# Kernel optimization log

Hardware: AMD Instinct MI355X
Metric: run time of the kernel (lower is better)

Reference implementation:

```python
import jax, jax.numpy as jnp
import numpy as np

KEY_CHANNELS = 256


def conv1x1_relu(x, w, b):
    # x: [B, Cin, H, W], w: [Cout, Cin], b: [Cout] -> [B, Cout, H, W]
    y = jnp.einsum('oc,bchw->bohw', w, x) + b[None, :, None, None]
    return jax.nn.relu(y)


def setup_inputs() -> dict:
    key = jax.random.key(0)
    ks = jax.random.split(key, 16)
    B, C, H, W = 8, 512, 128, 128
    Kc, Kp = KEY_CHANNELS, 150
    sc = lambda cin: 1.0 / np.sqrt(cin)
    return {
        'x': jax.random.normal(ks[0], (B, C, H, W), jnp.float32),
        'proxy': jax.random.normal(ks[1], (B, C, Kp, 1), jnp.float32),
        'w_fp1': jax.random.normal(ks[2], (Kc, C), jnp.float32) * sc(C),
        'b_fp1': jax.random.normal(ks[3], (Kc,), jnp.float32) * 0.1,
        'w_fp2': jax.random.normal(ks[4], (Kc, Kc), jnp.float32) * sc(Kc),
        'b_fp2': jax.random.normal(ks[5], (Kc,), jnp.float32) * 0.1,
        'w_fo1': jax.random.normal(ks[6], (Kc, C), jnp.float32) * sc(C),
        'b_fo1': jax.random.normal(ks[7], (Kc,), jnp.float32) * 0.1,
        'w_fo2': jax.random.normal(ks[8], (Kc, Kc), jnp.float32) * sc(Kc),
        'b_fo2': jax.random.normal(ks[9], (Kc,), jnp.float32) * 0.1,
        'w_fd': jax.random.normal(ks[10], (Kc, C), jnp.float32) * sc(C),
        'b_fd': jax.random.normal(ks[11], (Kc,), jnp.float32) * 0.1,
        'w_fu': jax.random.normal(ks[12], (C, Kc), jnp.float32) * sc(Kc),
        'b_fu': jax.random.normal(ks[13], (C,), jnp.float32) * 0.1,
    }


def reference(x, proxy, w_fp1, b_fp1, w_fp2, b_fp2, w_fo1, b_fo1,
              w_fo2, b_fo2, w_fd, b_fd, w_fu, b_fu):
    B, C, H, W = x.shape
    Kc = w_fp1.shape[0]
    # f_pixel: two 1x1 conv(+folded BN)+ReLU blocks -> query [B, HW, Kc]
    q = conv1x1_relu(conv1x1_relu(x, w_fp1, b_fp1), w_fp2, b_fp2)
    query = q.reshape(B, Kc, H * W).transpose(0, 2, 1)
    # f_object -> key [B, Kc, Kp]
    k = conv1x1_relu(conv1x1_relu(proxy, w_fo1, b_fo1), w_fo2, b_fo2)
    key = k.reshape(B, Kc, -1)
    # f_down -> value [B, Kp, Kc]
    v = conv1x1_relu(proxy, w_fd, b_fd)
    value = v.reshape(B, Kc, -1).transpose(0, 2, 1)
    # cross-attention: softmax(Q K^T / sqrt(Kc)) V
    sim = jnp.einsum('bnc,bck->bnk', query, key) * (Kc ** -0.5)
    sim = jax.nn.softmax(sim, axis=-1)
    context = jnp.einsum('bnk,bkc->bnc', sim, value)  # [B, HW, Kc]
    context = context.transpose(0, 2, 1).reshape(B, Kc, H, W)
    # f_up: 1x1 conv(+folded BN)+ReLU back to in_channels
    return conv1x1_relu(context, w_fu, b_fu)
```

## Files before the change

### kernel.cpp

```cpp
#include <hip/hip_runtime.h>
#include <hip/hip_bf16.h>


typedef __bf16 bf16x8 __attribute__((ext_vector_type(8)));
typedef float f32x4 __attribute__((ext_vector_type(4)));

#define AS1 __attribute__((address_space(1)))
#define AS3 __attribute__((address_space(3)))
#define MFMA_16x16x32(a, b, c) __builtin_amdgcn_mfma_f32_16x16x32_bf16((a), (b), (c), 0, 0, 0)

__device__ __forceinline__ unsigned short f2bf(float f) {
  union { float f; unsigned u; } x; x.f = f;
  unsigned r = (x.u + 0x7FFFu + ((x.u >> 16) & 1u)) >> 16;
  return (unsigned short)r;
}

__global__ __launch_bounds__(256) void cast_weights(
    const float* __restrict__ w1, const float* __restrict__ w2,
    const float* __restrict__ wu, unsigned short* __restrict__ W1b,
    unsigned short* __restrict__ W2b, unsigned short* __restrict__ Wub) {
  int i = blockIdx.x * 256 + threadIdx.x;
  if (i < 131072) W1b[i] = f2bf(w1[i]);
  else if (i < 196608) W2b[i - 131072] = f2bf(w2[i - 131072]);
  else if (i < 327680) Wub[i - 196608] = f2bf(wu[i - 196608]);
}

__global__ __launch_bounds__(256) void kv_kernel(
    const float* __restrict__ proxy,
    const float* __restrict__ w_fo1, const float* __restrict__ b_fo1,
    const float* __restrict__ w_fo2, const float* __restrict__ b_fo2,
    const float* __restrict__ w_fd, const float* __restrict__ b_fd,
    unsigned short* __restrict__ keyT, unsigned short* __restrict__ Vv) {
  __shared__ float cols[512][8];
  __shared__ float k1s[256][8];
  const int b = blockIdx.y;
  const int p0 = blockIdx.x * 8;
  const int t = threadIdx.x;
#pragma unroll
  for (int i = 0; i < 8; i++) {
    int idx = t + i * 256;
    int c = idx >> 2, q = idx & 3;
    int p = p0 + q * 2;
    float2 v = make_float2(0.f, 0.f);
    if (p < 150) v = *(const float2*)(proxy + ((size_t)b * 512 + c) * 150 + p);
    cols[c][q * 2 + 0] = v.x;
    cols[c][q * 2 + 1] = v.y;
  }
  __syncthreads();
  float accV[8], accK[8];
  {
    float bv = b_fd[t], bk = b_fo1[t];
#pragma unroll
    for (int px = 0; px < 8; px++) { accV[px] = bv; accK[px] = bk; }
  }
#define KV_FMA(j, wv_, wk_)                                      \
  { float4 ca = *(const float4*)&cols[c + j][0];                 \
    float4 cb = *(const float4*)&cols[c + j][4];                 \
    accV[0] += wv_ * ca.x; accV[1] += wv_ * ca.y;                \
    accV[2] += wv_ * ca.z; accV[3] += wv_ * ca.w;                \
    accV[4] += wv_ * cb.x; accV[5] += wv_ * cb.y;                \
    accV[6] += wv_ * cb.z; accV[7] += wv_ * cb.w;                \
    accK[0] += wk_ * ca.x; accK[1] += wk_ * ca.y;                \
    accK[2] += wk_ * ca.z; accK[3] += wk_ * ca.w;                \
    accK[4] += wk_ * cb.x; accK[5] += wk_ * cb.y;                \
    accK[6] += wk_ * cb.z; accK[7] += wk_ * cb.w; }
  for (int c = 0; c < 512; c += 4) {
    float4 wv4 = *(const float4*)(w_fd + (size_t)t * 512 + c);
    float4 wk4 = *(const float4*)(w_fo1 + (size_t)t * 512 + c);
    KV_FMA(0, wv4.x, wk4.x)
    KV_FMA(1, wv4.y, wk4.y)
    KV_FMA(2, wv4.z, wk4.z)
    KV_FMA(3, wv4.w, wk4.w)
  }
#pragma unroll
  for (int px = 0; px < 8; px++) {
    Vv[((size_t)b * 256 + t) * 160 + p0 + px] = f2bf(fmaxf(accV[px], 0.f));
    k1s[t][px] = fmaxf(accK[px], 0.f);
  }
  __syncthreads();
  float accY[8];
  {
    float by = b_fo2[t];
#pragma unroll
    for (int px = 0; px < 8; px++) accY[px] = by;
  }
#define KV_FMA2(j, wy_)                                          \
  { float4 ca = *(const float4*)&k1s[c + j][0];                  \
    float4 cb = *(const float4*)&k1s[c + j][4];                  \
    accY[0] += wy_ * ca.x; accY[1] += wy_ * ca.y;                \
    accY[2] += wy_ * ca.z; accY[3] += wy_ * ca.w;                \
    accY[4] += wy_ * cb.x; accY[5] += wy_ * cb.y;                \
    accY[6] += wy_ * cb.z; accY[7] += wy_ * cb.w; }
  for (int c = 0; c < 256; c += 4) {
    float4 wy4 = *(const float4*)(w_fo2 + (size_t)t * 256 + c);
    KV_FMA2(0, wy4.x)
    KV_FMA2(1, wy4.y)
    KV_FMA2(2, wy4.z)
    KV_FMA2(3, wy4.w)
  }
#pragma unroll
  for (int px = 0; px < 8; px++)
    keyT[((size_t)b * 160 + p0 + px) * 256 + t] = f2bf(fmaxf(accY[px], 0.f));
}

__global__ __launch_bounds__(256, 3) void gemm1_fused(
    const float* __restrict__ X, const unsigned short* __restrict__ Bt,
    const float* __restrict__ bias, unsigned short* __restrict__ Cq) {
  const int HW = 16384, K = 512, N = 256;
  __shared__ float Af[64 * 128];
  __shared__ unsigned short Bs[128 * 64];
  const int r = blockIdx.x;
  const int b = blockIdx.y;
  const int my = ((r >> 4) << 3) | (r & 7);
  const int nx = (r >> 3) & 1;
  const int m0 = my * 128, n0 = nx * 128;
  const int tid = threadIdx.x;
  const int w = tid >> 6, l = tid & 63;
  const int lr = l & 15, lg = l >> 4;
  const int wm = (w >> 1) * 64, wn = (w & 1) * 64;
  const float* Xb = X + (size_t)b * K * HW;
  const unsigned short* Btb = Bt + (size_t)n0 * K;
  const f32x4 zero = {0.f, 0.f, 0.f, 0.f};
  f32x4 acc[4][4];
#pragma unroll
  for (int m = 0; m < 4; m++)
#pragma unroll
    for (int n = 0; n < 4; n++) acc[m][n] = zero;

  const int arow = l >> 5, acol = l & 31;
  const int bsub = l >> 3, bcol = (l & 7) * 8;
  for (int kt = 0; kt < K; kt += 64) {
    __syncthreads();
#pragma unroll
    for (int i = 0; i < 8; i++) {
      const int rk = w * 16 + i * 2 + arow;
      const int s = (rk >> 3) & 7;
      __builtin_amdgcn_global_load_lds(
          (AS1 void*)(Xb + (size_t)(kt + rk) * HW + m0 + ((acol ^ s) << 2)),
          (AS3 void*)(Af + (w * 16 + i * 2) * 128), 16, 0, 0);
    }
#pragma unroll
    for (int i = 0; i < 4; i++) {
      __builtin_amdgcn_global_load_lds(
          (AS1 void*)(Btb + (size_t)(w * 32 + i * 8 + bsub) * K + kt + bcol),
          (AS3 void*)(Bs + (w * 32 + i * 8) * 64), 16, 0, 0);
    }
    __syncthreads();
#pragma unroll
    for (int ks = 0; ks < 2; ks++) {
      bf16x8 aF[4], bF[4];
      const int s = ks * 4 + lg;
#pragma unroll
      for (int m = 0; m < 4; m++) {
        const int p = wm + m * 16 + lr;
        const int cb = ((((p >> 2) ^ s) << 2) | (p & 3));
        bf16x8 a;
#pragma unroll
        for (int j = 0; j < 8; j++)
          a[j] = (__bf16)Af[(ks * 32 + lg * 8 + j) * 128 + cb];
        aF[m] = a;
      }
#pragma unroll
      for (int n = 0; n < 4; n++)
        bF[n] = *(const bf16x8*)(Bs + (wn + n * 16 + lr) * 64 + ks * 32 + lg * 8);
#pragma unroll
      for (int m = 0; m < 4; m++)
#pragma unroll
        for (int n = 0; n < 4; n++) acc[m][n] = MFMA_16x16x32(aF[m], bF[n], acc[m][n]);
    }
  }
  unsigned short* Cb = Cq + (size_t)b * HW * N;
#pragma unroll
  for (int m = 0; m < 4; m++) {
#pragma unroll
    for (int n = 0; n < 4; n++) {
      const int col = n0 + wn + n * 16 + lr;
      const float bc = bias[col];
#pragma unroll
      for (int r2 = 0; r2 < 4; r2++) {
        const int row = m0 + wm + m * 16 + lg * 4 + r2;
        Cb[(size_t)row * N + col] = f2bf(fmaxf(acc[m][n][r2] + bc, 0.f));
      }
    }
  }
}

template <int BIAS_ROW, int OUTF32, int COLOC>
__global__ __launch_bounds__(256, 4) void gemm_bt_relu(
    const unsigned short* __restrict__ A, const unsigned short* __restrict__ Bt,
    const float* __restrict__ bias, void* __restrict__ Cout,
    int M, int N, int K, long long sA, long long sB, long long sC) {
  __shared__ unsigned short As[128 * 64];
  __shared__ unsigned short Bs[128 * 64];
  int m0, n0, b;
  if (COLOC == 1) {
    const int g = blockIdx.x, x = g & 7, j = g >> 3;
    const int og = ((j >> 1) << 3) | x;
    n0 = (j & 1) * 128; m0 = (og & 127) * 128; b = og >> 7;
  } else if (COLOC == 2) {
    const int g = blockIdx.x, x = g & 7, j = g >> 3;
    const int og = ((j >> 2) << 3) | x;
    m0 = (j & 3) * 128; n0 = (og & 127) * 128; b = og >> 7;
  } else {
    b = blockIdx.z; m0 = blockIdx.x * 128; n0 = blockIdx.y * 128;
  }
  const int tid = threadIdx.x;
  const int w = tid >> 6, l = tid & 63;
  const int lr = l & 15, lg = l >> 4;
  const int wm = (w >> 1) * 64, wn = (w & 1) * 64;
  const unsigned short* Ab = A + (size_t)b * sA + (size_t)m0 * K;
  const unsigned short* Btb = Bt + (size_t)b * sB + (size_t)n0 * K;
  const f32x4 zero = {0.f, 0.f, 0.f, 0.f};
  f32x4 acc[4][4];
#pragma unroll
  for (int m = 0; m < 4; m++)
#pragma unroll
    for (int n = 0; n < 4; n++) acc[m][n] = zero;

  const int srow = w * 32 + (l >> 3);
  const int scol = (l & 7) * 8;
  for (int kt = 0; kt < K; kt += 64) {
    __syncthreads();
#pragma unroll
    for (int i = 0; i < 4; i++) {
      __builtin_amdgcn_global_load_lds(
          (AS1 void*)(Ab + (size_t)(srow + i * 8) * K + kt + scol),
          (AS3 void*)(As + (w * 32 + i * 8) * 64), 16, 0, 0);
      __builtin_amdgcn_global_load_lds(
          (AS1 void*)(Btb + (size_t)(srow + i * 8) * K + kt + scol),
          (AS3 void*)(Bs + (w * 32 + i * 8) * 64), 16, 0, 0);
    }
    __syncthreads();
#pragma unroll
    for (int ks = 0; ks < 2; ks++) {
      bf16x8 aF[4], bF[4];
#pragma unroll
      for (int m = 0; m < 4; m++)
        aF[m] = *(const bf16x8*)(As + (wm + m * 16 + lr) * 64 + ks * 32 + lg * 8);
#pragma unroll
      for (int n = 0; n < 4; n++)
        bF[n] = *(const bf16x8*)(Bs + (wn + n * 16 + lr) * 64 + ks * 32 + lg * 8);
#pragma unroll
      for (int m = 0; m < 4; m++)
#pragma unroll
        for (int n = 0; n < 4; n++) acc[m][n] = MFMA_16x16x32(aF[m], bF[n], acc[m][n]);
    }
  }
#pragma unroll
  for (int m = 0; m < 4; m++) {
#pragma unroll
    for (int n = 0; n < 4; n++) {
      const int col = n0 + wn + n * 16 + lr;
      const float bc = BIAS_ROW ? 0.f : bias[col];
#pragma unroll
      for (int r = 0; r < 4; r++) {
        const int row = m0 + wm + m * 16 + lg * 4 + r;
        float v = acc[m][n][r] + (BIAS_ROW ? bias[row] : bc);
        v = fmaxf(v, 0.f);
        if (OUTF32)
          ((float*)Cout)[(size_t)b * sC + (size_t)row * N + col] = v;
        else
          ((unsigned short*)Cout)[(size_t)b * sC + (size_t)row * N + col] = f2bf(v);
      }
    }
  }
}

__global__ __launch_bounds__(256, 4) void attn_kernel(
    const unsigned short* __restrict__ Q, const unsigned short* __restrict__ Kt,
    const unsigned short* __restrict__ Vv, unsigned short* __restrict__ ctxT) {
  const int HW = 16384;
  __shared__ unsigned short Pls[128 * 160];
  const int b = blockIdx.y;
  const int pix0 = blockIdx.x * 128;
  const int tid = threadIdx.x;
  const int w = tid >> 6, l = tid & 63;
  const int lr = l & 15, lg = l >> 4;
  const unsigned short* Qb = Q + ((size_t)b * HW + pix0 + w * 32) * 256;
  const unsigned short* Kb = Kt + (size_t)b * 160 * 256;
  const unsigned short* Vb = Vv + (size_t)b * 256 * 160;
  const f32x4 zero = {0.f, 0.f, 0.f, 0.f};

  f32x4 acc[2][10];
#pragma unroll
  for (int m = 0; m < 2; m++)
#pragma unroll
    for (int n = 0; n < 10; n++) acc[m][n] = zero;
#pragma unroll 2
  for (int ks = 0; ks < 8; ks++) {
    bf16x8 aF[2];
#pragma unroll
    for (int m = 0; m < 2; m++)
      aF[m] = *(const bf16x8*)(Qb + (size_t)(m * 16 + lr) * 256 + ks * 32 + lg * 8);
#pragma unroll
    for (int n = 0; n < 10; n++) {
      bf16x8 bF = *(const bf16x8*)(Kb + (size_t)(n * 16 + lr) * 256 + ks * 32 + lg * 8);
      acc[0][n] = MFMA_16x16x32(aF[0], bF, acc[0][n]);
      acc[1][n] = MFMA_16x16x32(aF[1], bF, acc[1][n]);
    }
  }
  const float scale = 0.0625f;
#pragma unroll
  for (int m = 0; m < 2; m++) {
#pragma unroll
    for (int r = 0; r < 4; r++) {
      float lm = -1e30f;
#pragma unroll
      for (int n = 0; n < 10; n++) {
        float v = acc[m][n][r] * scale;
        acc[m][n][r] = v;
        if (n * 16 + lr < 150) lm = fmaxf(lm, v);
      }
#pragma unroll
      for (int msk = 1; msk <= 8; msk <<= 1) lm = fmaxf(lm, __shfl_xor(lm, msk, 64));
      float s = 0.f;
#pragma unroll
      for (int n = 0; n < 10; n++) {
        float p = (n * 16 + lr < 150) ? __expf(acc[m][n][r] - lm) : 0.f;
        acc[m][n][r] = p;
        s += p;
      }
#pragma unroll
      for (int msk = 1; msk <= 8; msk <<= 1) s += __shfl_xor(s, msk, 64);
      float inv = 1.f / s;
      const int row = w * 32 + m * 16 + lg * 4 + r;
      const unsigned sw = (unsigned)(row & 7) << 4;
#pragma unroll
      for (int n = 0; n < 10; n++) {
        unsigned boff = (unsigned)row * 320 + (unsigned)(n * 16 + lr) * 2;
        *(unsigned short*)((char*)Pls + (boff ^ sw)) = f2bf(acc[m][n][r] * inv);
      }
    }
  }
  __syncthreads();
  unsigned short* Cb = ctxT + ((size_t)b * HW + pix0 + w * 32) * 256;
#pragma unroll
  for (int half = 0; half < 2; half++) {
    f32x4 acc2[2][8];
#pragma unroll
    for (int m = 0; m < 2; m++)
#pragma unroll
      for (int n = 0; n < 8; n++) acc2[m][n] = zero;
    for (int ks = 0; ks < 5; ks++) {
      bf16x8 aP[2];
#pragma unroll
      for (int m = 0; m < 2; m++) {
        const int row = w * 32 + m * 16 + lr;
        unsigned boff = (unsigned)row * 320 + (unsigned)(ks * 64 + lg * 16);
        aP[m] = *(const bf16x8*)((const char*)Pls + (boff ^ ((unsigned)(row & 7) << 4)));
      }
#pragma unroll
      for (int n = 0; n < 8; n++) {
        const int ch = half * 128 + n * 16 + lr;
        bf16x8 bV = *(const bf16x8*)(Vb + (size_t)ch * 160 + ks * 32 + lg * 8);
        acc2[0][n] = MFMA_16x16x32(aP[0], bV, acc2[0][n]);
        acc2[1][n] = MFMA_16x16x32(aP[1], bV, acc2[1][n]);
      }
    }
#pragma unroll
    for (int m = 0; m < 2; m++)
#pragma unroll
      for (int n = 0; n < 8; n++)
#pragma unroll
        for (int r = 0; r < 4; r++)
          Cb[(size_t)(m * 16 + lg * 4 + r) * 256 + half * 128 + n * 16 + lr] =
              f2bf(acc2[m][n][r]);
  }
}

extern "C" void kernel_launch(void* const* d_in, const int* in_sizes, int n_in,
                              void* d_out, int out_size, void* d_ws, size_t ws_size,
                              hipStream_t stream) {
  (void)in_sizes; (void)n_in; (void)out_size;
  const float* x     = (const float*)d_in[0];
  const float* proxy = (const float*)d_in[1];
  const float* w_fp1 = (const float*)d_in[2];
  const float* b_fp1 = (const float*)d_in[3];
  const float* w_fp2 = (const float*)d_in[4];
  const float* b_fp2 = (const float*)d_in[5];
  const float* w_fo1 = (const float*)d_in[6];
  const float* b_fo1 = (const float*)d_in[7];
  const float* w_fo2 = (const float*)d_in[8];
  const float* b_fo2 = (const float*)d_in[9];
  const float* w_fd  = (const float*)d_in[10];
  const float* b_fd  = (const float*)d_in[11];
  const float* w_fu  = (const float*)d_in[12];
  const float* b_fu  = (const float*)d_in[13];

  char* ws = (char*)d_ws;
  unsigned short* W1b  = (unsigned short*)(ws + 0);
  unsigned short* W2b  = (unsigned short*)(ws + 262144);
  unsigned short* Wub  = (unsigned short*)(ws + 393216);
  unsigned short* keyT = (unsigned short*)(ws + 655360);
  unsigned short* Vv   = (unsigned short*)(ws + 1310720);
  unsigned short* bufA = (unsigned short*)(ws + 2097152);
  unsigned short* bufB = (unsigned short*)(ws + 2097152 + 134217728);
  if (ws_size < 203423744) return;

  dim3 blk(256);
  cast_weights<<<1280, blk, 0, stream>>>(w_fp1, w_fp2, w_fu, W1b, W2b, Wub);
  kv_kernel<<<dim3(20, 8), blk, 0, stream>>>(proxy, w_fo1, b_fo1, w_fo2, b_fo2,
                                             w_fd, b_fd, keyT, Vv);
  gemm1_fused<<<dim3(256, 8), blk, 0, stream>>>(x, W1b, b_fp1, bufB);
  gemm_bt_relu<0, 0, 1><<<2048, blk, 0, stream>>>(
      bufB, W2b, b_fp2, bufA, 16384, 256, 256,
      (long long)16384 * 256, 0, (long long)16384 * 256);
  attn_kernel<<<dim3(128, 8), blk, 0, stream>>>(bufA, keyT, Vv, bufB);
  gemm_bt_relu<1, 1, 2><<<4096, blk, 0, stream>>>(
      Wub, bufB, b_fu, d_out, 512, 16384, 256,
      0, (long long)16384 * 256, (long long)512 * 16384);
}
```

Baseline: 371.7 us.

## Replace f_up GEMM with weight-stationary streaming kernel over pixel tiles

The final f_up 1x1 conv now runs in a dedicated kernel. Each block loads a 128x256 bf16 weight slab into swizzled LDS once via global_load_lds, then loops over 8 pixel tiles of 128, reading context fragments straight from global memory into MFMAs and writing fused bias+ReLU fp32 output. This avoids re-staging A and B tiles through LDS for every output tile and cuts the grid from 4096 to 512 blocks. The trade-off is that B operands are uncached, unshared global loads per wave, and the loop has less latency hiding.

```diff
diff --git a/kernel.cpp b/kernel.cpp
--- a/kernel.cpp
+++ b/kernel.cpp
@@ -197,10 +197,6 @@
     const int g = blockIdx.x, x = g & 7, j = g >> 3;
     const int og = ((j >> 1) << 3) | x;
     n0 = (j & 1) * 128; m0 = (og & 127) * 128; b = og >> 7;
-  } else if (COLOC == 2) {
-    const int g = blockIdx.x, x = g & 7, j = g >> 3;
-    const int og = ((j >> 2) << 3) | x;
-    m0 = (j & 3) * 128; n0 = (og & 127) * 128; b = og >> 7;
   } else {
     b = blockIdx.z; m0 = blockIdx.x * 128; n0 = blockIdx.y * 128;
   }
@@ -365,6 +361,81 @@
         for (int r = 0; r < 4; r++)
           Cb[(size_t)(m * 16 + lg * 4 + r) * 256 + half * 128 + n * 16 + lr] =
               f2bf(acc2[m][n][r]);
+  }
+}
+
+__global__ __launch_bounds__(256, 2) void gup_stream(
+    const unsigned short* __restrict__ Wu, const unsigned short* __restrict__ ctxT,
+    const float* __restrict__ bu, float* __restrict__ Out) {
+  const int HW = 16384;
+  __shared__ __align__(16) unsigned short Als[128 * 256];
+  const int g = blockIdx.x;
+  const int xcd = g & 7, j = g >> 3;
+  const int mp = j & 3, pairhi = j >> 2;
+  const int pair = (pairhi << 3) | xcd;
+  const int b = pair >> 4, pg = pair & 15;
+  const int m0 = mp * 128;
+  const int tid = (int)threadIdx.x;
+  const int w = tid >> 6, l = tid & 63;
+  const int lr = l & 15, lg = l >> 4;
+  const f32x4 zero = {0.f, 0.f, 0.f, 0.f};
+
+  {
+    const int lco = l >> 5;
+    const int t16 = l & 31;
+#pragma unroll
+    for (int i = 0; i < 16; i++) {
+      const int op = w * 16 + i;
+      const int co = op * 2 + lco;
+      const int src16 = t16 ^ (co & 7);
+      __builtin_amdgcn_global_load_lds(
+          (AS1 void*)(Wu + (size_t)(m0 + co) * 256 + src16 * 8),
+          (AS3 void*)((char*)Als + op * 1024), 16, 0, 0);
+    }
+  }
+  __syncthreads();
+
+  const int wm = w * 32;
+  const unsigned short* Cb = ctxT + (size_t)b * HW * 256;
+  float* Ob = Out + (size_t)b * 512 * HW + (size_t)m0 * HW;
+
+#pragma unroll 1
+  for (int t = 0; t < 8; t++) {
+    const int pix0 = pg * 1024 + t * 128;
+    f32x4 acc[2][8];
+#pragma unroll
+    for (int m = 0; m < 2; m++)
+#pragma unroll
+      for (int n = 0; n < 8; n++) acc[m][n] = zero;
+#pragma unroll
+    for (int ks = 0; ks < 8; ks++) {
+      bf16x8 aF[2];
+#pragma unroll
+      for (int m = 0; m < 2; m++) {
+        const int co = wm + m * 16 + lr;
+        const unsigned boff =
+            ((unsigned)co << 9) + ((unsigned)(((ks << 2) + lg) ^ (co & 7)) << 4);
+        aF[m] = *(const bf16x8*)((const char*)Als + boff);
+      }
+#pragma unroll
+      for (int n = 0; n < 8; n++) {
+        bf16x8 bF = *(const bf16x8*)(Cb + (size_t)(pix0 + n * 16 + lr) * 256 +
+                                     ks * 32 + lg * 8);
+        acc[0][n] = MFMA_16x16x32(aF[0], bF, acc[0][n]);
+        acc[1][n] = MFMA_16x16x32(aF[1], bF, acc[1][n]);
+      }
+    }
+#pragma unroll
+    for (int m = 0; m < 2; m++) {
+#pragma unroll
+      for (int r = 0; r < 4; r++) {
+        const int co = wm + m * 16 + lg * 4 + r;
+        const float bb = bu[m0 + co];
+#pragma unroll
+        for (int n = 0; n < 8; n++)
+          Ob[(size_t)co * HW + pix0 + n * 16 + lr] = fmaxf(acc[m][n][r] + bb, 0.f);
+      }
+    }
   }
 }
 
@@ -406,7 +477,5 @@
       bufB, W2b, b_fp2, bufA, 16384, 256, 256,
       (long long)16384 * 256, 0, (long long)16384 * 256);
   attn_kernel<<<dim3(128, 8), blk, 0, stream>>>(bufA, keyT, Vv, bufB);
-  gemm_bt_relu<1, 1, 2><<<4096, blk, 0, stream>>>(
-      Wub, bufB, b_fu, d_out, 512, 16384, 256,
-      0, (long long)16384 * 256, (long long)512 * 16384);
-}
+  gup_stream<<<512, blk, 0, stream>>>(Wub, bufB, b_fu, (float*)d_out);
+}
```

New measurement: 472.5 us. 27.1% more time.

## Fuse the two f_pixel 1x1 conv GEMMs into one head kernel via LDS

Applied to the files above, without the earlier changes.

Replaces the separate first-layer GEMM and second-layer GEMM with one kernel. Each block computes all 256 channels of layer one for 128 pixels, stages the bf16 result in swizzled shared memory, then runs the 256x256 second GEMM directly from LDS, with W2 fragments read from global memory. This removes the global write and re-read of the intermediate query buffer and one launch. In exchange it uses more registers and 64KB of LDS, so only 2 blocks fit per CU, and the W2 reads are uncached global loads in the inner loop.

```diff
diff --git a/kernel.cpp b/kernel.cpp
--- a/kernel.cpp
+++ b/kernel.cpp
@@ -103,84 +103,125 @@
     keyT[((size_t)b * 160 + p0 + px) * 256 + t] = f2bf(fmaxf(accY[px], 0.f));
 }
 
-__global__ __launch_bounds__(256, 3) void gemm1_fused(
-    const float* __restrict__ X, const unsigned short* __restrict__ Bt,
-    const float* __restrict__ bias, unsigned short* __restrict__ Cq) {
-  const int HW = 16384, K = 512, N = 256;
-  __shared__ float Af[64 * 128];
-  __shared__ unsigned short Bs[128 * 64];
-  const int r = blockIdx.x;
-  const int b = blockIdx.y;
-  const int my = ((r >> 4) << 3) | (r & 7);
-  const int nx = (r >> 3) & 1;
-  const int m0 = my * 128, n0 = nx * 128;
-  const int tid = threadIdx.x;
+__global__ __launch_bounds__(256, 2) void head_kernel(
+    const float* __restrict__ X, const unsigned short* __restrict__ W1,
+    const float* __restrict__ b1, const unsigned short* __restrict__ W2,
+    const float* __restrict__ b2, unsigned short* __restrict__ q2out) {
+  const int HW = 16384, K = 512;
+  __shared__ __align__(16) char smem[65536];
+  float* Af = (float*)smem;
+  unsigned short* Bs = (unsigned short*)(smem + 32768);
+  const int bid = blockIdx.x;
+  const int b = bid >> 7, pt = bid & 127;
+  const int p0 = pt * 128;
+  const int tid = (int)threadIdx.x;
   const int w = tid >> 6, l = tid & 63;
   const int lr = l & 15, lg = l >> 4;
-  const int wm = (w >> 1) * 64, wn = (w & 1) * 64;
-  const float* Xb = X + (size_t)b * K * HW;
-  const unsigned short* Btb = Bt + (size_t)n0 * K;
   const f32x4 zero = {0.f, 0.f, 0.f, 0.f};
-  f32x4 acc[4][4];
+
+  const int wm = (w >> 1) * 64;
+  const int wn = (w & 1) * 128;
+  f32x4 acc[4][8];
 #pragma unroll
   for (int m = 0; m < 4; m++)
 #pragma unroll
-    for (int n = 0; n < 4; n++) acc[m][n] = zero;
-
-  const int arow = l >> 5, acol = l & 31;
-  const int bsub = l >> 3, bcol = (l & 7) * 8;
-  for (int kt = 0; kt < K; kt += 64) {
-    __syncthreads();
-#pragma unroll
-    for (int i = 0; i < 8; i++) {
-      const int rk = w * 16 + i * 2 + arow;
-      const int s = (rk >> 3) & 7;
-      __builtin_amdgcn_global_load_lds(
-          (AS1 void*)(Xb + (size_t)(kt + rk) * HW + m0 + ((acol ^ s) << 2)),
-          (AS3 void*)(Af + (w * 16 + i * 2) * 128), 16, 0, 0);
-    }
-#pragma unroll
-    for (int i = 0; i < 4; i++) {
-      __builtin_amdgcn_global_load_lds(
-          (AS1 void*)(Btb + (size_t)(w * 32 + i * 8 + bsub) * K + kt + bcol),
-          (AS3 void*)(Bs + (w * 32 + i * 8) * 64), 16, 0, 0);
-    }
-    __syncthreads();
-#pragma unroll
-    for (int ks = 0; ks < 2; ks++) {
-      bf16x8 aF[4], bF[4];
-      const int s = ks * 4 + lg;
-#pragma unroll
-      for (int m = 0; m < 4; m++) {
-        const int p = wm + m * 16 + lr;
-        const int cb = ((((p >> 2) ^ s) << 2) | (p & 3));
-        bf16x8 a;
-#pragma unroll
-        for (int j = 0; j < 8; j++)
-          a[j] = (__bf16)Af[(ks * 32 + lg * 8 + j) * 128 + cb];
-        aF[m] = a;
-      }
-#pragma unroll
-      for (int n = 0; n < 4; n++)
-        bF[n] = *(const bf16x8*)(Bs + (wn + n * 16 + lr) * 64 + ks * 32 + lg * 8);
-#pragma unroll
-      for (int m = 0; m < 4; m++)
-#pragma unroll
-        for (int n = 0; n < 4; n++) acc[m][n] = MFMA_16x16x32(aF[m], bF[n], acc[m][n]);
-    }
-  }
-  unsigned short* Cb = Cq + (size_t)b * HW * N;
-#pragma unroll
-  for (int m = 0; m < 4; m++) {
-#pragma unroll
-    for (int n = 0; n < 4; n++) {
-      const int col = n0 + wn + n * 16 + lr;
-      const float bc = bias[col];
-#pragma unroll
-      for (int r2 = 0; r2 < 4; r2++) {
-        const int row = m0 + wm + m * 16 + lg * 4 + r2;
-        Cb[(size_t)row * N + col] = f2bf(fmaxf(acc[m][n][r2] + bc, 0.f));
-      }
+    for (int n = 0; n < 8; n++) acc[m][n] = zero;
+  {
+    const float* Xb = X + (size_t)b * K * HW;
+    const int arow = l >> 5, acol = l & 31;
+    const int bsub = l >> 3, bcol = (l & 7) * 8;
+#pragma unroll 1
+    for (int kt = 0; kt < K; kt += 64) {
+      __syncthreads();
+#pragma unroll
+      for (int i = 0; i < 8; i++) {
+        const int rk = w * 16 + i * 2 + arow;
+        const int s = (rk >> 3) & 7;
+        __builtin_amdgcn_global_load_lds(
+            (AS1 void*)(Xb + (size_t)(kt + rk) * HW + p0 + ((acol ^ s) << 2)),
+            (AS3 void*)(Af + (w * 16 + i * 2) * 128), 16, 0, 0);
+      }
+#pragma unroll
+      for (int i = 0; i < 8; i++) {
+        __builtin_amdgcn_global_load_lds(
+            (AS1 void*)(W1 + (size_t)(w * 64 + i * 8 + bsub) * K + kt + bcol),
+            (AS3 void*)(Bs + (w * 64 + i * 8) * 64), 16, 0, 0);
+      }
+      __syncthreads();
+#pragma unroll
+      for (int ks = 0; ks < 2; ks++) {
+        const int s = ks * 4 + lg;
+        bf16x8 aF[4];
+#pragma unroll
+        for (int m = 0; m < 4; m++) {
+          const int p = wm + m * 16 + lr;
+          const int cb = (((p >> 2) ^ s) << 2) | (p & 3);
+          bf16x8 a;
+#pragma unroll
+          for (int j = 0; j < 8; j++)
+            a[j] = (__bf16)Af[(ks * 32 + lg * 8 + j) * 128 + cb];
+          aF[m] = a;
+        }
+#pragma unroll
+        for (int n = 0; n < 8; n++) {
+          bf16x8 bF = *(const bf16x8*)(Bs + (wn + n * 16 + lr) * 64 + ks * 32 + lg * 8);
+#pragma unroll
+          for (int m = 0; m < 4; m++) acc[m][n] = MFMA_16x16x32(aF[m], bF, acc[m][n]);
+        }
+      }
+    }
+  }
+  __syncthreads();
+#pragma unroll
+  for (int n = 0; n < 8; n++) {
+    const int ch = wn + n * 16 + lr;
+    const float bb = b1[ch];
+#pragma unroll
+    for (int m = 0; m < 4; m++)
+#pragma unroll
+      for (int r = 0; r < 4; r++) {
+        const int px = wm + m * 16 + lg * 4 + r;
+        const unsigned boff =
+            ((unsigned)px * 512 + (unsigned)ch * 2) ^ (((unsigned)px & 7u) << 4);
+        *(unsigned short*)(smem + boff) = f2bf(fmaxf(acc[m][n][r] + bb, 0.f));
+      }
+  }
+  __syncthreads();
+  {
+    const int pbase = w * 32;
+    f32x4 acc2[2][16];
+#pragma unroll
+    for (int m = 0; m < 2; m++)
+#pragma unroll
+      for (int n = 0; n < 16; n++) acc2[m][n] = zero;
+#pragma unroll
+    for (int ks = 0; ks < 8; ks++) {
+      bf16x8 aF[2];
+#pragma unroll
+      for (int m = 0; m < 2; m++) {
+        const int p = pbase + m * 16 + lr;
+        const unsigned boff = ((unsigned)p * 512 + (unsigned)(ks * 64 + lg * 16)) ^
+                              (((unsigned)p & 7u) << 4);
+        aF[m] = *(const bf16x8*)(smem + boff);
+      }
+#pragma unroll
+      for (int n = 0; n < 16; n++) {
+        bf16x8 bF = *(const bf16x8*)(W2 + (size_t)(n * 16 + lr) * 256 + ks * 32 + lg * 8);
+        acc2[0][n] = MFMA_16x16x32(aF[0], bF, acc2[0][n]);
+        acc2[1][n] = MFMA_16x16x32(aF[1], bF, acc2[1][n]);
+      }
+    }
+    unsigned short* Cb = q2out + ((size_t)b * HW + p0 + pbase) * 256;
+#pragma unroll
+    for (int n = 0; n < 16; n++) {
+      const int ch = n * 16 + lr;
+      const float bb = b2[ch];
+#pragma unroll
+      for (int m = 0; m < 2; m++)
+#pragma unroll
+        for (int r = 0; r < 4; r++)
+          Cb[(size_t)(m * 16 + lg * 4 + r) * 256 + ch] =
+              f2bf(fmaxf(acc2[m][n][r] + bb, 0.f));
     }
   }
 }
@@ -193,11 +234,7 @@
   __shared__ unsigned short As[128 * 64];
   __shared__ unsigned short Bs[128 * 64];
   int m0, n0, b;
-  if (COLOC == 1) {
-    const int g = blockIdx.x, x = g & 7, j = g >> 3;
-    const int og = ((j >> 1) << 3) | x;
-    n0 = (j & 1) * 128; m0 = (og & 127) * 128; b = og >> 7;
-  } else if (COLOC == 2) {
+  if (COLOC == 2) {
     const int g = blockIdx.x, x = g & 7, j = g >> 3;
     const int og = ((j >> 2) << 3) | x;
     m0 = (j & 3) * 128; n0 = (og & 127) * 128; b = og >> 7;
@@ -394,17 +431,14 @@
   unsigned short* keyT = (unsigned short*)(ws + 655360);
   unsigned short* Vv   = (unsigned short*)(ws + 1310720);
   unsigned short* bufA = (unsigned short*)(ws + 2097152);
-  unsigned short* bufB = (unsigned short*)(ws + 2097152 + 134217728);
-  if (ws_size < 203423744) return;
+  unsigned short* bufB = (unsigned short*)(ws + 2097152 + 67108864);
+  if (ws_size < 2097152 + 2 * 67108864) return;
 
   dim3 blk(256);
   cast_weights<<<1280, blk, 0, stream>>>(w_fp1, w_fp2, w_fu, W1b, W2b, Wub);
   kv_kernel<<<dim3(20, 8), blk, 0, stream>>>(proxy, w_fo1, b_fo1, w_fo2, b_fo2,
                                              w_fd, b_fd, keyT, Vv);
-  gemm1_fused<<<dim3(256, 8), blk, 0, stream>>>(x, W1b, b_fp1, bufB);
-  gemm_bt_relu<0, 0, 1><<<2048, blk, 0, stream>>>(
-      bufB, W2b, b_fp2, bufA, 16384, 256, 256,
-      (long long)16384 * 256, 0, (long long)16384 * 256);
+  head_kernel<<<1024, blk, 0, stream>>>(x, W1b, b_fp1, W2b, b_fp2, bufA);
   attn_kernel<<<dim3(128, 8), blk, 0, stream>>>(bufA, keyT, Vv, bufB);
   gemm_bt_relu<1, 1, 2><<<4096, blk, 0, stream>>>(
       Wub, bufB, b_fu, d_out, 512, 16384, 256,
```

New measurement: 392.3 us. 1.06x slower.
